# Optimization experiments

Measured on AMD Instinct MI355X. Metric: run time of the kernel, lower is better.

Reference implementation:

```python
import jax, jax.numpy as jnp
import numpy as np

# Fixed Db4 filters (non-learnable buffers in the original module)
_H = np.array([-0.010597401785069032, 0.032883011666982945, 0.030841381835560764,
               -0.18703481171888114, -0.02798376941698385, 0.6308807679295904,
               0.7148465705529155, 0.2303778133088964], dtype=np.float32)
_G = np.array([(-1.0) ** k * v for k, v in enumerate(_H[::-1])], dtype=np.float32)

LEVELS = 5  # max(1, floor(log2(256)) - 3)


def _dwt_level(x, filt):
    """reflect-pad left (K-1), depthwise cross-correlation, stride-2 decimation.
    Equivalent to torch: F.pad(x,(K-1,0),'reflect') -> conv1d(groups=C) -> [..., ::2].
    Fused into a single strided conv since out[::2] == stride-2 conv from offset 0."""
    K = filt.shape[0]
    C = x.shape[1]
    xp = jnp.pad(x, ((0, 0), (0, 0), (K - 1, 0)), mode='reflect')
    w = jnp.broadcast_to(filt.reshape(1, 1, K), (C, 1, K))  # (C,1,K) depthwise
    return jax.lax.conv_general_dilated(
        xp, w, window_strides=(2,), padding='VALID',
        dimension_numbers=('NCH', 'OIH', 'NCH'), feature_group_count=C)


def _forward(x, db4_low, db4_high):
    approx = x
    details = []
    for _ in range(LEVELS):
        low = _dwt_level(approx, db4_low)
        high = _dwt_level(approx, db4_high)
        details.append(high)
        approx = low
    Fd = approx                    # final approximation  (B,C,S/32)
    Ft = details[-1]               # (B,C,S/32)
    Fa = details[-2]               # (B,C,S/16)
    Fb = details[-3]               # (B,C,S/8)
    Fg = details[-4]               # (B,C,S/4)
    FR = jnp.concatenate([Fd, Ft, Fa, Fb, Fg], axis=2)
    return (Fd, Ft, Fa, Fb, Fg, FR)


def setup_inputs() -> dict:
    key = jax.random.key(0)
    x = jax.random.normal(key, (64, 64, 16384), dtype=jnp.float32)
    return {"x": x, "db4_low": jnp.asarray(_H), "db4_high": jnp.asarray(_G)}


def reference(x, db4_low, db4_high):
    return _forward(x, db4_low, db4_high)
```

## Files before the change

kernel.cpp:

```cpp
#include <hip/hip_runtime.h>


static constexpr int SLEN = 16384;

typedef float f32x4 __attribute__((ext_vector_type(4)));

__device__ __forceinline__ int swz4(int f) {
    const int s = f >> 2;
    return (s ^ ((s >> 3) & 7)) << 2;
}
__device__ __forceinline__ int swz1(int f) {
    const int s = f >> 2;
    return (((s ^ ((s >> 3) & 7)) << 2) | (f & 3));
}

__device__ __forceinline__ float dotH(const float* w) {
    float s =      -0.010597401785069032f * w[0];
    s = fmaf( 0.032883011666982945f, w[1], s);
    s = fmaf( 0.030841381835560764f, w[2], s);
    s = fmaf(-0.18703481171888114f,  w[3], s);
    s = fmaf(-0.02798376941698385f,  w[4], s);
    s = fmaf( 0.6308807679295904f,   w[5], s);
    s = fmaf( 0.7148465705529155f,   w[6], s);
    s = fmaf( 0.2303778133088964f,   w[7], s);
    return s;
}
__device__ __forceinline__ float dotG(const float* w) {
    float s =       0.2303778133088964f * w[0];
    s = fmaf(-0.7148465705529155f,   w[1], s);
    s = fmaf( 0.6308807679295904f,   w[2], s);
    s = fmaf( 0.02798376941698385f,  w[3], s);
    s = fmaf(-0.18703481171888114f,  w[4], s);
    s = fmaf(-0.030841381835560764f, w[5], s);
    s = fmaf( 0.032883011666982945f, w[6], s);
    s = fmaf( 0.010597401785069032f, w[7], s);
    return s;
}

__device__ __forceinline__ void loadw16g(const float* __restrict__ src, int q, float* w) {
    if (q == 0) {
#pragma unroll
        for (int i = 0; i < 16; ++i) { int m = i - 8; m = (m < 0) ? -m : m; w[i] = src[m]; }
    } else {
        const float4 v0 = *(const float4*)(src + 8 * q - 8);
        const float4 v1 = *(const float4*)(src + 8 * q - 4);
        const float4 v2 = *(const float4*)(src + 8 * q);
        const float4 v3 = *(const float4*)(src + 8 * q + 4);
        w[0]  = v0.x; w[1]  = v0.y; w[2]  = v0.z; w[3]  = v0.w;
        w[4]  = v1.x; w[5]  = v1.y; w[6]  = v1.z; w[7]  = v1.w;
        w[8]  = v2.x; w[9]  = v2.y; w[10] = v2.z; w[11] = v2.w;
        w[12] = v3.x; w[13] = v3.y; w[14] = v3.z; w[15] = v3.w;
    }
}

__device__ __forceinline__ void lw16s(const float* __restrict__ base, int foff, float* w) {
#pragma unroll
    for (int j = 0; j < 4; ++j) {
        const float4 v = *(const float4*)(base + swz4(foff + 4 * j));
        w[4*j+0] = v.x; w[4*j+1] = v.y; w[4*j+2] = v.z; w[4*j+3] = v.w;
    }
}
__device__ __forceinline__ void lw16s_q0(const float* __restrict__ base, float* w) {
#pragma unroll
    for (int i = 0; i < 16; ++i) { int m = i - 8; m = (m < 0) ? -m : m; w[i] = base[swz1(m)]; }
}

__device__ __forceinline__ void ntst4(float* p, float a0, float a1, float a2, float a3) {
    f32x4 v; v.x = a0; v.y = a1; v.z = a2; v.w = a3;
    __builtin_nontemporal_store(v, (f32x4*)p);
}

__device__ __forceinline__ void barrier_lds() {
    asm volatile("s_waitcnt lgkmcnt(0)" ::: "memory");
    __builtin_amdgcn_s_barrier();
    asm volatile("" ::: "memory");
}

__global__ __launch_bounds__(256, 6)
void dwt5_kernel(const float* __restrict__ x, float* __restrict__ out)
{
    __shared__ float buf[6336];
    const int bid = blockIdx.x;
    const int r   = bid >> 1;
    const int h   = bid & 1;
    const int tid = threadIdx.x;

    const float* __restrict__ xr = x + (size_t)r * SLEN;
    const size_t frBase = (size_t)33554432 + (size_t)r * 8192;

    const int A1s = h ? 3976 : 0;
    const int A2s = h ? 1992 : 0;
    const int A3s = h ? 1000 : 0;
    const int A4s = h ?  504 : 0;
    constexpr int REG2 = 4224;
    constexpr int REG4 = 2048;

    {
        const int g1lo = A1s >> 2;
        const int g1hi = h ? 2048 : 1024;
#pragma unroll
        for (int jj = 0; jj < 5; ++jj) {
            const int g = g1lo + tid + jj * 256;
            if (g < g1hi) {
                float w[16];
                loadw16g(xr, g, w);
                const float a0 = dotH(w + 1), a1 = dotH(w + 3), a2 = dotH(w + 5), a3 = dotH(w + 7);
                *(float4*)(buf + swz4(4 * g - A1s)) = make_float4(a0, a1, a2, a3);
            }
        }
    }
    barrier_lds();

    {
        const int g2lo = A2s >> 2;
        const int g2hi = h ? 1024 : 512;
        const int gd   = h ? 512 : 0;
        float* __restrict__ hi1 = out + (size_t)16777216 + (size_t)r * 4096;
        float* __restrict__ hi2 = out + frBase + 4096;
#pragma unroll
        for (int jj = 0; jj < 3; ++jj) {
            const int g = g2lo + tid + jj * 256;
            if (g < g2hi) {
                float w[16];
                if (g == 0) lw16s_q0(buf, w);
                else        lw16s(buf, 8 * g - 8 - A1s, w);
                const float a0 = dotH(w + 1), a1 = dotH(w + 3), a2 = dotH(w + 5), a3 = dotH(w + 7);
                *(float4*)(buf + REG2 + swz4(4 * g - A2s)) = make_float4(a0, a1, a2, a3);
                if (g >= gd) {
                    const float d0 = dotG(w + 1), d1 = dotG(w + 3), d2 = dotG(w + 5), d3 = dotG(w + 7);
                    ntst4(hi1 + 4 * g, d0, d1, d2, d3);
                    ntst4(hi2 + 4 * g, d0, d1, d2, d3);
                }
            }
        }
    }
    barrier_lds();

    {
        const int g3lo = A3s >> 2;
        const int g3hi = h ? 512 : 256;
        const int gd   = h ? 256 : 0;
        float* __restrict__ hi1 = out + (size_t)8388608 + (size_t)r * 2048;
        float* __restrict__ hi2 = out + frBase + 2048;
#pragma unroll
        for (int jj = 0; jj < 2; ++jj) {
            const int g = g3lo + tid + jj * 256;
            if (g < g3hi) {
                float w[16];
                if (g == 0) lw16s_q0(buf + REG2, w);
                else        lw16s(buf + REG2, 8 * g - 8 - A2s, w);
                const float a0 = dotH(w + 1), a1 = dotH(w + 3), a2 = dotH(w + 5), a3 = dotH(w + 7);
                *(float4*)(buf + swz4(4 * g - A3s)) = make_float4(a0, a1, a2, a3);
                if (g >= gd) {
                    const float d0 = dotG(w + 1), d1 = dotG(w + 3), d2 = dotG(w + 5), d3 = dotG(w + 7);
                    ntst4(hi1 + 4 * g, d0, d1, d2, d3);
                    ntst4(hi2 + 4 * g, d0, d1, d2, d3);
                }
            }
        }
    }
    barrier_lds();

    {
        const int g4lo = A4s >> 2;
        const int g4hi = h ? 256 : 128;
        const int gd   = h ? 128 : 0;
        float* __restrict__ hi1 = out + (size_t)4194304 + (size_t)r * 1024;
        float* __restrict__ hi2 = out + frBase + 1024;
        const int g = g4lo + tid;
        if (g < g4hi) {
            float w[16];
            if (g == 0) lw16s_q0(buf, w);
            else        lw16s(buf, 8 * g - 8 - A3s, w);
            const float a0 = dotH(w + 1), a1 = dotH(w + 3), a2 = dotH(w + 5), a3 = dotH(w + 7);
            *(float4*)(buf + REG4 + swz4(4 * g - A4s)) = make_float4(a0, a1, a2, a3);
            if (g >= gd) {
                const float d0 = dotG(w + 1), d1 = dotG(w + 3), d2 = dotG(w + 5), d3 = dotG(w + 7);
                ntst4(hi1 + 4 * g, d0, d1, d2, d3);
                ntst4(hi2 + 4 * g, d0, d1, d2, d3);
            }
        }
    }
    barrier_lds();

    {
        const int g5lo = h ? 64 : 0;
        const int g = g5lo + tid;
        if (g < g5lo + 64) {
            float w[16];
            if (g == 0) lw16s_q0(buf + REG4, w);
            else        lw16s(buf + REG4, 8 * g - 8 - A4s, w);
            const float a0 = dotH(w + 1), a1 = dotH(w + 3), a2 = dotH(w + 5), a3 = dotH(w + 7);
            const float d0 = dotG(w + 1), d1 = dotG(w + 3), d2 = dotG(w + 5), d3 = dotG(w + 7);
            ntst4(out + (size_t)r * 512 + 4 * g,                   a0, a1, a2, a3);
            ntst4(out + frBase + 4 * g,                            a0, a1, a2, a3);
            ntst4(out + (size_t)2097152 + (size_t)r * 512 + 4 * g, d0, d1, d2, d3);
            ntst4(out + frBase + 512 + 4 * g,                      d0, d1, d2, d3);
        }
    }
}

extern "C" void kernel_launch(void* const* d_in, const int* in_sizes, int n_in,
                              void* d_out, int out_size, void* d_ws, size_t ws_size,
                              hipStream_t stream) {
    const float* x = (const float*)d_in[0];
    float* out = (float*)d_out;
    dwt5_kernel<<<8192, 256, 0, stream>>>(x, out);
}
```

Measured before the change: 87.53 us.

## Compose two DWT levels into 22-tap filters and split rows into quarters

Folds pairs of levels into combined 22-tap low-low and high-low filters computed at compile time. Level 2 is then computed straight from global input, and level 4 straight from level 2 in LDS, with reflect-boundary special cases handled separately. Each row is now split across four blocks instead of two, which shrinks shared memory and raises the occupancy target to 8. The aim is fewer LDS round trips and barriers and more parallelism, at the cost of redundant halo reads and extra FMAs per output.

```diff
diff --git a/kernel.cpp b/kernel.cpp
--- a/kernel.cpp
+++ b/kernel.cpp
@@ -2,8 +2,27 @@
 
 
 static constexpr int SLEN = 16384;
-
 typedef float f32x4 __attribute__((ext_vector_type(4)));
+
+constexpr double Hd[8] = {-0.010597401785069032, 0.032883011666982945, 0.030841381835560764,
+                          -0.18703481171888114, -0.02798376941698385, 0.6308807679295904,
+                          0.7148465705529155, 0.2303778133088964};
+constexpr double Gd[8] = { 0.2303778133088964, -0.7148465705529155, 0.6308807679295904,
+                           0.02798376941698385, -0.18703481171888114, -0.030841381835560764,
+                           0.032883011666982945, 0.010597401785069032};
+
+struct C22 { float c[22]; };
+constexpr C22 comp22(const double* o, const double* in) {
+    C22 r{};
+    double acc[22] = {};
+    for (int j = 0; j < 8; ++j)
+        for (int k = 0; k < 8; ++k)
+            acc[2*j + k] += o[j] * in[k];
+    for (int i = 0; i < 22; ++i) r.c[i] = (float)acc[i];
+    return r;
+}
+constexpr C22 CLL = comp22(Hd, Hd);
+constexpr C22 CHL = comp22(Gd, Hd);
 
 __device__ __forceinline__ int swz4(int f) {
     const int s = f >> 2;
@@ -37,26 +56,94 @@
     return s;
 }
 
-__device__ __forceinline__ void loadw16g(const float* __restrict__ src, int q, float* w) {
-    if (q == 0) {
-#pragma unroll
-        for (int i = 0; i < 16; ++i) { int m = i - 8; m = (m < 0) ? -m : m; w[i] = src[m]; }
-    } else {
-        const float4 v0 = *(const float4*)(src + 8 * q - 8);
-        const float4 v1 = *(const float4*)(src + 8 * q - 4);
-        const float4 v2 = *(const float4*)(src + 8 * q);
-        const float4 v3 = *(const float4*)(src + 8 * q + 4);
-        w[0]  = v0.x; w[1]  = v0.y; w[2]  = v0.z; w[3]  = v0.w;
-        w[4]  = v1.x; w[5]  = v1.y; w[6]  = v1.z; w[7]  = v1.w;
-        w[8]  = v2.x; w[9]  = v2.y; w[10] = v2.z; w[11] = v2.w;
-        w[12] = v3.x; w[13] = v3.y; w[14] = v3.z; w[15] = v3.w;
+#define COMP_BODY(LOADEXPR)                                              \
+    _Pragma("unroll")                                                    \
+    for (int t = 0; t < 4; ++t) { accA[t] = 0.f; accD[t] = 0.f; }        \
+    _Pragma("unroll")                                                    \
+    for (int s = 0; s < 10; ++s) {                                       \
+        const float4 v = (LOADEXPR);                                     \
+        const float ve[4] = {v.x, v.y, v.z, v.w};                        \
+        _Pragma("unroll")                                                \
+        for (int e = 0; e < 4; ++e) {                                    \
+            _Pragma("unroll")                                            \
+            for (int t = 0; t < 4; ++t) {                                \
+                const int i = 4*s + e - 4*t - 3;                         \
+                if (i >= 0 && i < 22) {                                  \
+                    accA[t] = fmaf(CLL.c[i], ve[e], accA[t]);            \
+                    accD[t] = fmaf(CHL.c[i], ve[e], accD[t]);            \
+                }                                                        \
+            }                                                            \
+        }                                                                \
+    }
+
+__device__ __forceinline__ void comp4g(const float* __restrict__ wp,
+                                       float* accA, float* accD) {
+    COMP_BODY(*(const float4*)(wp + 4*s))
+}
+__device__ __forceinline__ void comp4l(const float* __restrict__ base, int rel,
+                                       float* accA, float* accD) {
+    COMP_BODY(*(const float4*)(base + swz4(rel + 4*s)))
+}
+
+template<int Q>
+__device__ __forceinline__ void bndA2(const float* __restrict__ xr,
+                                      float* accA, float* accD) {
+    float a1v[15];
+#pragma unroll
+    for (int m = 0; m < 15; ++m) {
+        float s = 0.f;
+#pragma unroll
+        for (int k = 0; k < 8; ++k) {
+            int ix = 2*m + k - 7; ix = ix < 0 ? -ix : ix;
+            s = fmaf((float)Hd[k], xr[ix], s);
+        }
+        a1v[m] = s;
+    }
+#pragma unroll
+    for (int t = 0; t < 4; ++t) {
+        float sa = 0.f, sd = 0.f;
+#pragma unroll
+        for (int j = 0; j < 8; ++j) {
+            int ix = 2*(4*Q + t) + j - 7; ix = ix < 0 ? -ix : ix;
+            const float v = a1v[ix];
+            sa = fmaf((float)Hd[j], v, sa);
+            sd = fmaf((float)Gd[j], v, sd);
+        }
+        accA[t] = sa; accD[t] = sd;
+    }
+}
+template<int P>
+__device__ __forceinline__ void bndA4(const float* __restrict__ a2b,
+                                      float* accA, float* accD) {
+    float a3v[15];
+#pragma unroll
+    for (int m = 0; m < 15; ++m) {
+        float s = 0.f;
+#pragma unroll
+        for (int k = 0; k < 8; ++k) {
+            int ix = 2*m + k - 7; ix = ix < 0 ? -ix : ix;
+            s = fmaf((float)Hd[k], a2b[swz1(ix)], s);
+        }
+        a3v[m] = s;
+    }
+#pragma unroll
+    for (int t = 0; t < 4; ++t) {
+        float sa = 0.f, sd = 0.f;
+#pragma unroll
+        for (int j = 0; j < 8; ++j) {
+            int ix = 2*(4*P + t) + j - 7; ix = ix < 0 ? -ix : ix;
+            const float v = a3v[ix];
+            sa = fmaf((float)Hd[j], v, sa);
+            sd = fmaf((float)Gd[j], v, sd);
+        }
+        accA[t] = sa; accD[t] = sd;
     }
 }
 
 __device__ __forceinline__ void lw16s(const float* __restrict__ base, int foff, float* w) {
 #pragma unroll
     for (int j = 0; j < 4; ++j) {
-        const float4 v = *(const float4*)(base + swz4(foff + 4 * j));
+        const float4 v = *(const float4*)(base + swz4(foff + 4*j));
         w[4*j+0] = v.x; w[4*j+1] = v.y; w[4*j+2] = v.z; w[4*j+3] = v.w;
     }
 }
@@ -76,60 +163,46 @@
     asm volatile("" ::: "memory");
 }
 
-__global__ __launch_bounds__(256, 6)
+__global__ __launch_bounds__(256, 8)
 void dwt5_kernel(const float* __restrict__ x, float* __restrict__ out)
 {
-    __shared__ float buf[6336];
+    __shared__ float buf[1376];
+    float* const a2b = buf;
+    float* const a4b = buf + 1088;
+
     const int bid = blockIdx.x;
-    const int r   = bid >> 1;
-    const int h   = bid & 1;
+    const int r   = bid >> 2;
+    const int qd  = bid & 3;
     const int tid = threadIdx.x;
 
     const float* __restrict__ xr = x + (size_t)r * SLEN;
     const size_t frBase = (size_t)33554432 + (size_t)r * 8192;
 
-    const int A1s = h ? 3976 : 0;
-    const int A2s = h ? 1992 : 0;
-    const int A3s = h ? 1000 : 0;
-    const int A4s = h ?  504 : 0;
-    constexpr int REG2 = 4224;
-    constexpr int REG4 = 2048;
+    const int A2s = qd ? 1024*qd - 56 : 0;
+    const int A4s = qd ? 256*qd  - 8  : 0;
 
     {
-        const int g1lo = A1s >> 2;
-        const int g1hi = h ? 2048 : 1024;
-#pragma unroll
-        for (int jj = 0; jj < 5; ++jj) {
-            const int g = g1lo + tid + jj * 256;
-            if (g < g1hi) {
-                float w[16];
-                loadw16g(xr, g, w);
-                const float a0 = dotH(w + 1), a1 = dotH(w + 3), a2 = dotH(w + 5), a3 = dotH(w + 7);
-                *(float4*)(buf + swz4(4 * g - A1s)) = make_float4(a0, a1, a2, a3);
-            }
-        }
-    }
-    barrier_lds();
-
-    {
-        const int g2lo = A2s >> 2;
-        const int g2hi = h ? 1024 : 512;
-        const int gd   = h ? 512 : 0;
         float* __restrict__ hi1 = out + (size_t)16777216 + (size_t)r * 4096;
         float* __restrict__ hi2 = out + frBase + 4096;
-#pragma unroll
-        for (int jj = 0; jj < 3; ++jj) {
-            const int g = g2lo + tid + jj * 256;
-            if (g < g2hi) {
-                float w[16];
-                if (g == 0) lw16s_q0(buf, w);
-                else        lw16s(buf, 8 * g - 8 - A1s, w);
-                const float a0 = dotH(w + 1), a1 = dotH(w + 3), a2 = dotH(w + 5), a3 = dotH(w + 7);
-                *(float4*)(buf + REG2 + swz4(4 * g - A2s)) = make_float4(a0, a1, a2, a3);
-                if (g >= gd) {
-                    const float d0 = dotG(w + 1), d1 = dotG(w + 3), d2 = dotG(w + 5), d3 = dotG(w + 7);
-                    ntst4(hi1 + 4 * g, d0, d1, d2, d3);
-                    ntst4(hi2 + 4 * g, d0, d1, d2, d3);
+        const int q0  = A2s >> 2;
+        const int qhi = 256*(qd+1);
+        const int gd  = 256*qd;
+#pragma unroll
+        for (int jj = 0; jj < 2; ++jj) {
+            const int q = q0 + tid + jj*256;
+            if (q < qhi) {
+                float accA[4], accD[4];
+                if (qd == 0 && q < 2) {
+                    if (q == 0) bndA2<0>(xr, accA, accD);
+                    else        bndA2<1>(xr, accA, accD);
+                } else {
+                    comp4g(xr + 16*q - 24, accA, accD);
+                }
+                *(float4*)(a2b + swz4(4*q - A2s)) =
+                    make_float4(accA[0], accA[1], accA[2], accA[3]);
+                if (q >= gd) {
+                    ntst4(hi1 + 4*q, accD[0], accD[1], accD[2], accD[3]);
+                    ntst4(hi2 + 4*q, accD[0], accD[1], accD[2], accD[3]);
                 }
             }
         }
@@ -137,66 +210,52 @@
     barrier_lds();
 
     {
-        const int g3lo = A3s >> 2;
-        const int g3hi = h ? 512 : 256;
-        const int gd   = h ? 256 : 0;
-        float* __restrict__ hi1 = out + (size_t)8388608 + (size_t)r * 2048;
-        float* __restrict__ hi2 = out + frBase + 2048;
-#pragma unroll
-        for (int jj = 0; jj < 2; ++jj) {
-            const int g = g3lo + tid + jj * 256;
-            if (g < g3hi) {
-                float w[16];
-                if (g == 0) lw16s_q0(buf + REG2, w);
-                else        lw16s(buf + REG2, 8 * g - 8 - A2s, w);
-                const float a0 = dotH(w + 1), a1 = dotH(w + 3), a2 = dotH(w + 5), a3 = dotH(w + 7);
-                *(float4*)(buf + swz4(4 * g - A3s)) = make_float4(a0, a1, a2, a3);
-                if (g >= gd) {
-                    const float d0 = dotG(w + 1), d1 = dotG(w + 3), d2 = dotG(w + 5), d3 = dotG(w + 7);
-                    ntst4(hi1 + 4 * g, d0, d1, d2, d3);
-                    ntst4(hi2 + 4 * g, d0, d1, d2, d3);
+        if (tid < 128) {
+            const int p = 128*qd + tid;
+            float* __restrict__ hi1 = out + (size_t)8388608 + (size_t)r * 2048;
+            float* __restrict__ hi2 = out + frBase + 2048;
+            float w[16];
+            if (p == 0) lw16s_q0(a2b, w);
+            else        lw16s(a2b, 8*p - 8 - A2s, w);
+            const float d0 = dotG(w+1), d1 = dotG(w+3), d2 = dotG(w+5), d3 = dotG(w+7);
+            ntst4(hi1 + 4*p, d0, d1, d2, d3);
+            ntst4(hi2 + 4*p, d0, d1, d2, d3);
+        } else {
+            const int t2  = tid - 128;
+            const int p   = (A4s >> 2) + t2;
+            const int phi = 64*(qd+1);
+            if (p < phi) {
+                float accA[4], accD[4];
+                if (qd == 0 && p < 2) {
+                    if (p == 0) bndA4<0>(a2b, accA, accD);
+                    else        bndA4<1>(a2b, accA, accD);
+                } else {
+                    comp4l(a2b, 16*p - 24 - A2s, accA, accD);
+                }
+                *(float4*)(a4b + swz4(4*p - A4s)) =
+                    make_float4(accA[0], accA[1], accA[2], accA[3]);
+                if (p >= 64*qd) {
+                    float* __restrict__ hi1 = out + (size_t)4194304 + (size_t)r * 1024;
+                    float* __restrict__ hi2 = out + frBase + 1024;
+                    ntst4(hi1 + 4*p, accD[0], accD[1], accD[2], accD[3]);
+                    ntst4(hi2 + 4*p, accD[0], accD[1], accD[2], accD[3]);
                 }
             }
         }
     }
     barrier_lds();
 
-    {
-        const int g4lo = A4s >> 2;
-        const int g4hi = h ? 256 : 128;
-        const int gd   = h ? 128 : 0;
-        float* __restrict__ hi1 = out + (size_t)4194304 + (size_t)r * 1024;
-        float* __restrict__ hi2 = out + frBase + 1024;
-        const int g = g4lo + tid;
-        if (g < g4hi) {
-            float w[16];
-            if (g == 0) lw16s_q0(buf, w);
-            else        lw16s(buf, 8 * g - 8 - A3s, w);
-            const float a0 = dotH(w + 1), a1 = dotH(w + 3), a2 = dotH(w + 5), a3 = dotH(w + 7);
-            *(float4*)(buf + REG4 + swz4(4 * g - A4s)) = make_float4(a0, a1, a2, a3);
-            if (g >= gd) {
-                const float d0 = dotG(w + 1), d1 = dotG(w + 3), d2 = dotG(w + 5), d3 = dotG(w + 7);
-                ntst4(hi1 + 4 * g, d0, d1, d2, d3);
-                ntst4(hi2 + 4 * g, d0, d1, d2, d3);
-            }
-        }
-    }
-    barrier_lds();
-
-    {
-        const int g5lo = h ? 64 : 0;
-        const int g = g5lo + tid;
-        if (g < g5lo + 64) {
-            float w[16];
-            if (g == 0) lw16s_q0(buf + REG4, w);
-            else        lw16s(buf + REG4, 8 * g - 8 - A4s, w);
-            const float a0 = dotH(w + 1), a1 = dotH(w + 3), a2 = dotH(w + 5), a3 = dotH(w + 7);
-            const float d0 = dotG(w + 1), d1 = dotG(w + 3), d2 = dotG(w + 5), d3 = dotG(w + 7);
-            ntst4(out + (size_t)r * 512 + 4 * g,                   a0, a1, a2, a3);
-            ntst4(out + frBase + 4 * g,                            a0, a1, a2, a3);
-            ntst4(out + (size_t)2097152 + (size_t)r * 512 + 4 * g, d0, d1, d2, d3);
-            ntst4(out + frBase + 512 + 4 * g,                      d0, d1, d2, d3);
-        }
+    if (tid < 32) {
+        const int q5 = 32*qd + tid;
+        float w[16];
+        if (q5 == 0) lw16s_q0(a4b, w);
+        else         lw16s(a4b, 8*q5 - 8 - A4s, w);
+        const float a0 = dotH(w+1), a1 = dotH(w+3), a2v = dotH(w+5), a3v = dotH(w+7);
+        const float d0 = dotG(w+1), d1 = dotG(w+3), d2v = dotG(w+5), d3v = dotG(w+7);
+        ntst4(out + (size_t)r*512 + 4*q5,                   a0, a1, a2v, a3v);
+        ntst4(out + frBase + 4*q5,                          a0, a1, a2v, a3v);
+        ntst4(out + (size_t)2097152 + (size_t)r*512 + 4*q5, d0, d1, d2v, d3v);
+        ntst4(out + frBase + 512 + 4*q5,                    d0, d1, d2v, d3v);
     }
 }
 
@@ -205,5 +264,5 @@
                               hipStream_t stream) {
     const float* x = (const float*)d_in[0];
     float* out = (float*)d_out;
-    dwt5_kernel<<<8192, 256, 0, stream>>>(x, out);
-}
+    dwt5_kernel<<<16384, 256, 0, stream>>>(x, out);
+}
```

New measurement: 137.8 us. +57.4%, slower.
